# Optimization experiments

Hardware: AMD Instinct MI355X
Metric: run time of the kernel (lower is better)

The kernel has to match this reference:

```python
import jax, jax.numpy as jnp
import numpy as np

B, N, T, IN_DIM, OUT_DIM = 16, 500, 12, 2, 2
H, D, K, NH, NBLOCKS, T_OUT, GDEP = 64, 64, 10, 24, 2, 12, 2
H2 = 2 * H


def setup_inputs():
    key = jax.random.key(0)
    ks = iter(jax.random.split(key, 64))

    def rn(shape, s=1.0):
        return jax.random.normal(next(ks), shape, dtype=jnp.float32) * s

    def z(*shape):
        return jnp.zeros(shape, jnp.float32)

    sI = 1.0 / np.sqrt(IN_DIM)
    sH = 1.0 / np.sqrt(H)
    sH2 = 1.0 / np.sqrt(H2)
    sD = 1.0 / np.sqrt(D)
    adj = jax.random.uniform(next(ks), (N, N), dtype=jnp.float32)
    inp = {
        'x': rn((B, N, T, IN_DIM)),
        'weather': rn((B, T, 4)),
        'geo_adj': adj / adj.sum(1, keepdims=True),
        'fcx_W': rn((IN_DIM, H), sI), 'fcx_b': z(H),
        'env_cb': rn((K, D)), 'nodes_cb': rn((N, D)),
        'w_v': rn((D, K), sD), 'w_k': rn((D, D), sD), 'w_q': rn((D, D), sD),
        'core_W': rn((H, H * H), sH), 'core_b': z(H * H),
        'tcnN_Win': rn((K, H2, H2), sH2), 'tcnN_bin': z(K, H2),
        'tcnN_Wf': rn((K, NBLOCKS, 2, H2, H2), sH2), 'tcnN_bf': z(K, NBLOCKS, H2),
        'tcnN_Wg': rn((K, NBLOCKS, 2, H2, H2), sH2), 'tcnN_bg': z(K, NBLOCKS, H2),
        'tcnN_Wout': rn((K, H2, H), sH2), 'tcnN_bout': z(K, H),
        'tcnP_Win': rn((K, H2, H2), sH2), 'tcnP_bin': z(K, H2),
        'tcnP_Wf': rn((K, NBLOCKS, 2, H2, H2), sH2), 'tcnP_bf': z(K, NBLOCKS, H2),
        'tcnP_Wg': rn((K, NBLOCKS, 2, H2, H2), sH2), 'tcnP_bg': z(K, NBLOCKS, H2),
        'tcnP_Wout': rn((K, H2, H), sH2), 'tcnP_bout': z(K, H),
        'bn1_g': jnp.ones((H,), jnp.float32), 'bn1_b': z(H),
        'bnP_g': jnp.ones((H,), jnp.float32), 'bnP_b': z(H),
        'gcn1_W': rn((H, H), sH), 'gcn1_b': z(H),
        'gcn2_W': rn((H, H), sH), 'gcn2_b': z(H),
        'gcnp_W': rn((H, H), sH), 'gcnp_b': z(H),
        'nv_p1': rn((2 * NH, H)), 'nv_p2': rn((N, H)), 'nv_p3': rn((N, H)),
        'nv_pk': rn((H, H, H), sH),
        'out_W1': rn((T_OUT, H, 100), sH), 'out_b1': z(T_OUT, 100),
        'out_W2': rn((T_OUT, 100, OUT_DIM), 0.1), 'out_b2': z(T_OUT, OUT_DIM),
        't_pos': jax.random.randint(next(ks), (B, T, 2), 0, 7),
        'ind': jax.random.randint(next(ks), (B, T, 2), 0, 7),
    }
    return inp


def _tstep_emb(t, dim):
    half = dim // 2
    freqs = jnp.exp(-jnp.log(10000.0) * jnp.arange(half, dtype=jnp.float32) / half)
    a = t.astype(jnp.float32)[:, None] * freqs[None]
    return jnp.concatenate([jnp.cos(a), jnp.sin(a)], -1)


def _conv2(h, W, b, d):
    # causal kernel-2 dilated conv over time: h [B,N,T,C], W [2,C,Co] -> [B,N,T-d,Co]
    return (jnp.einsum('bntc,co->bnto', h[:, :, :-d], W[0])
            + jnp.einsum('bntc,co->bnto', h[:, :, d:], W[1]) + b)


def _tcn(xin, Win, bin_, Wf, bf, Wg, bg, Wout, bout):
    # gated dilated TCN (Graph-WaveNet style), per node over time
    h = jnp.einsum('bntc,co->bnto', xin, Win) + bin_
    for l in range(Wf.shape[0]):
        d = 2 ** l
        f = jnp.tanh(_conv2(h, Wf[l], bf[l], d))
        g = jax.nn.sigmoid(_conv2(h, Wg[l], bg[l], d))
        h = f * g + h[:, :, d:, :]
    return jnp.einsum('bntc,ch->bnth', h, Wout) + bout


def _bn(h, g, b):
    # BatchNorm1d over channels, stats over (batch, nodes); training mode
    mu = h.mean((0, 1))
    var = h.var((0, 1))
    return g * (h - mu) * jax.lax.rsqrt(var + 1e-5) + b


def _gcn(h, adj, W, b):
    # multi-hop diffusion: sum_{k=0..GDEP} A^k h, then linear
    eq = 'nm,bmh->bnh' if adj.ndim == 2 else 'bnm,bmh->bnh'
    acc, zt = h, h
    for _ in range(GDEP):
        zt = jnp.einsum(eq, adj, zt)
        acc = acc + zt
    return jnp.einsum('bnh,ho->bno', acc, W) + b


def _forward(x, weather, geo_adj, fcx_W, fcx_b, env_cb, nodes_cb, w_v, w_k, w_q,
             core_W, core_b,
             tcnN_Win, tcnN_bin, tcnN_Wf, tcnN_bf, tcnN_Wg, tcnN_bg, tcnN_Wout, tcnN_bout,
             tcnP_Win, tcnP_bin, tcnP_Wf, tcnP_bf, tcnP_Wg, tcnP_bg, tcnP_Wout, tcnP_bout,
             bn1_g, bn1_b, bnP_g, bnP_b, gcn1_W, gcn1_b, gcn2_W, gcn2_b, gcnp_W, gcnp_b,
             nv_p1, nv_p2, nv_p3, nv_pk, out_W1, out_b1, out_W2, out_b2, t_pos, ind):
    scale = 1.0 / jnp.sqrt(jnp.float32(D))
    ind_p = jnp.where(ind[:, :, 0] <= 4, ind[:, :, 1], NH - 1 + ind[:, :, 1])
    tp = jnp.where(t_pos[:, :, 0] <= 4, t_pos[:, :, 1], NH - 1 + t_pos[:, :, 1])
    t_emb = _tstep_emb(tp.reshape(-1), H).reshape(B, T, H)

    # codebook attention -> hard cluster assignment (gumbel softmax, straight-through)
    mat_v = env_cb @ w_v
    mat_k = env_cb @ w_k
    mat_q = nodes_cb @ w_q
    scores = jax.nn.softmax((mat_q @ mat_k.T) * scale, axis=1)
    logits = scores @ mat_v                                   # [N,K]
    gn = jax.random.gumbel(jax.random.key(42), logits.shape, dtype=logits.dtype)
    y_soft = jax.nn.softmax(logits + gn, axis=1)
    hard = jax.nn.one_hot(jnp.argmax(y_soft, axis=1), K, dtype=y_soft.dtype)
    mask = y_soft + jax.lax.stop_gradient(hard - y_soft)      # [N,K] one-hot fwd

    x_emb = jnp.einsum('bnti,ih->bnth', x, fcx_W) + fcx_b
    total_x = jnp.concatenate(
        [x_emb, jnp.broadcast_to(t_emb[:, None], (B, N, T, H))], -1)  # [B,N,T,2H]

    unbias = jnp.zeros((B, N, H), total_x.dtype)
    h_prev = jnp.zeros((B, N, H), total_x.dtype)
    for i in range(K):  # small fixed cluster count
        m = mask[:, i]
        xm = total_x * m[None, :, None, None]
        hn = _tcn(xm[:, :, 1:], tcnN_Win[i], tcnN_bin[i], tcnN_Wf[i], tcnN_bf[i],
                  tcnN_Wg[i], tcnN_bg[i], tcnN_Wout[i], tcnN_bout[i])[:, :, 0, :]
        hp = _tcn(xm[:, :, :-1], tcnP_Win[i], tcnP_bin[i], tcnP_Wf[i], tcnP_bf[i],
                  tcnP_Wg[i], tcnP_bg[i], tcnP_Wout[i], tcnP_bout[i])[:, :, 0, :]
        unbias = unbias + m[None, :, None] * hn
        h_prev = h_prev + m[None, :, None] * hp

    unbias = _bn(unbias, bn1_g, bn1_b)
    h_prev = _bn(h_prev, bnP_g, bnP_b)

    h1 = _gcn(h_prev, geo_adj, gcn1_W, gcn1_b)
    core = (t_emb[:, T - 1] @ core_W + core_b).reshape(B, H, H)
    causal = jax.nn.softmax(jnp.einsum('bnh,bhk,bmk->bnm', unbias, core, h_prev), axis=-1)
    h2 = _gcn(unbias, causal, gcn2_W, gcn2_b)

    te = nv_p1[ind_p[:, -(T - 1)]]                            # [B,H]
    adp = jnp.einsum('ai,ijk->ajk', te, nv_pk)
    adp = jnp.einsum('bj,ajk->abk', nv_p2, adp)
    adp = jnp.einsum('ck,abk->abc', nv_p3, adp)
    adp = jax.nn.softmax(jax.nn.relu(adp), axis=2)            # [B,N,N]
    h3 = _gcn(unbias, adp, gcnp_W, gcnp_b)

    cur_h = h1 + h2 + h3
    hmid = jax.nn.elu(jnp.einsum('bnh,thf->bntf', cur_h, out_W1) + out_b1)
    return jnp.einsum('bntf,tfo->bnto', hmid, out_W2) + out_b2  # [B,N,T_OUT,OUT_DIM]


def reference(x, weather, geo_adj, fcx_W, fcx_b, env_cb, nodes_cb, w_v, w_k, w_q,
              core_W, core_b,
              tcnN_Win, tcnN_bin, tcnN_Wf, tcnN_bf, tcnN_Wg, tcnN_bg, tcnN_Wout, tcnN_bout,
              tcnP_Win, tcnP_bin, tcnP_Wf, tcnP_bf, tcnP_Wg, tcnP_bg, tcnP_Wout, tcnP_bout,
              bn1_g, bn1_b, bnP_g, bnP_b, gcn1_W, gcn1_b, gcn2_W, gcn2_b, gcnp_W, gcnp_b,
              nv_p1, nv_p2, nv_p3, nv_pk, out_W1, out_b1, out_W2, out_b2, t_pos, ind):
    return _forward(x, weather, geo_adj, fcx_W, fcx_b, env_cb, nodes_cb, w_v, w_k, w_q,
                    core_W, core_b,
                    tcnN_Win, tcnN_bin, tcnN_Wf, tcnN_bf, tcnN_Wg, tcnN_bg, tcnN_Wout, tcnN_bout,
                    tcnP_Win, tcnP_bin, tcnP_Wf, tcnP_bf, tcnP_Wg, tcnP_bg, tcnP_Wout, tcnP_bout,
                    bn1_g, bn1_b, bnP_g, bnP_b, gcn1_W, gcn1_b, gcn2_W, gcn2_b, gcnp_W, gcnp_b,
                    nv_p1, nv_p2, nv_p3, nv_pk, out_W1, out_b1, out_W2, out_b2, t_pos, ind)
```

## Files before the change

kernel.cpp:

```cpp
#include <hip/hip_runtime.h>
#include <hip/hip_bf16.h>
#include <math.h>

#define B_ 16
#define N_ 500
#define T_ 12
#define K_ 10
#define NROWS (B_*N_)
#define TROWS 6
#define NTCN2 2688

__device__ __forceinline__ unsigned rotl32(unsigned v, int r){ return (v<<r)|(v>>(32-r)); }

__device__ __forceinline__ void threefry2x32(unsigned k0, unsigned k1,
                                             unsigned c0, unsigned c1,
                                             unsigned &o0, unsigned &o1){
  unsigned ks2 = k0 ^ k1 ^ 0x1BD11BDAu;
  unsigned x0 = c0 + k0, x1 = c1 + k1;
#define TF_R(r) { x0 += x1; x1 = rotl32(x1,(r)); x1 ^= x0; }
  TF_R(13) TF_R(15) TF_R(26) TF_R(6)
  x0 += k1;  x1 += ks2 + 1u;
  TF_R(17) TF_R(29) TF_R(16) TF_R(24)
  x0 += ks2; x1 += k0 + 2u;
  TF_R(13) TF_R(15) TF_R(26) TF_R(6)
  x0 += k0;  x1 += k1 + 3u;
  TF_R(17) TF_R(29) TF_R(16) TF_R(24)
  x0 += k1;  x1 += ks2 + 4u;
  TF_R(13) TF_R(15) TF_R(26) TF_R(6)
  x0 += ks2; x1 += k0 + 5u;
#undef TF_R
  o0 = x0; o1 = x1;
}

__device__ __forceinline__ float gumbel_at(unsigned idx){
  unsigned b0, b1;
  threefry2x32(0u, 42u, 0u, idx, b0, b1);
  unsigned bits = b0 ^ b1;
  float u = __uint_as_float((bits >> 9) | 0x3f800000u) - 1.0f;
  u = fmaxf(u, 1.17549435e-38f);
  return -logf(-logf(u));
}

__global__ __launch_bounds__(256) void k_matq(const float* __restrict__ nodes_cb,
                                              const float* __restrict__ w_q,
                                              float* __restrict__ matq){
  int idx = blockIdx.x*256 + threadIdx.x;
  if (idx >= N_*64) return;
  int n = idx >> 6, d = idx & 63;
  float a = 0.f;
  for (int c = 0; c < 64; ++c) a += nodes_cb[n*64+c] * w_q[c*64+d];
  matq[idx] = a;
}

__global__ __launch_bounds__(256) void k_route(const float* __restrict__ env_cb,
                                               const float* __restrict__ w_v,
                                               const float* __restrict__ w_k,
                                               const float* __restrict__ matq,
                                               int* __restrict__ node_list,
                                               int* __restrict__ off){
  __shared__ float smk[K_*64];
  __shared__ float smv[K_*K_];
  __shared__ int sroute[N_];
  int tid = threadIdx.x;
  for (int idx = tid; idx < K_*64; idx += 256){
    int kk = idx >> 6, d = idx & 63;
    float a = 0.f;
    for (int c = 0; c < 64; ++c) a += env_cb[kk*64+c] * w_k[c*64+d];
    smk[idx] = a;
  }
  for (int idx = tid; idx < K_*K_; idx += 256){
    int kk = idx / K_, j = idx % K_;
    float a = 0.f;
    for (int c = 0; c < 64; ++c) a += env_cb[kk*64+c] * w_v[c*K_+j];
    smv[idx] = a;
  }
  __syncthreads();
  for (int n = tid; n < N_; n += 256){
    float s[K_];
    float mx = -1e30f;
    for (int j = 0; j < K_; ++j){
      float a = 0.f;
      for (int d = 0; d < 64; ++d) a += matq[n*64+d]*smk[j*64+d];
      s[j] = a * 0.125f;
      mx = fmaxf(mx, s[j]);
    }
    float sum = 0.f;
    for (int j = 0; j < K_; ++j){ s[j] = expf(s[j]-mx); sum += s[j]; }
    float inv = 1.f/sum;
    int best = 0; float bestv = -1e30f;
    for (int j2 = 0; j2 < K_; ++j2){
      float lg = 0.f;
      for (int j = 0; j < K_; ++j) lg += s[j]*inv*smv[j*K_+j2];
      float tot = lg + gumbel_at((unsigned)(n*K_+j2));
      if (tot > bestv){ bestv = tot; best = j2; }
    }
    sroute[n] = best;
  }
  __syncthreads();
  if (tid == 0){
    int cnt[K_]; for (int j=0;j<K_;++j) cnt[j]=0;
    for (int n=0;n<N_;++n) cnt[sroute[n]]++;
    int acc=0;
    for (int j=0;j<K_;++j){ off[j]=acc; acc+=cnt[j]; }
    off[K_]=acc;
    int pos[K_]; for (int j=0;j<K_;++j) pos[j]=off[j];
    for (int n=0;n<N_;++n) node_list[pos[sroute[n]]++] = n;
    int* chunkOff = off + 16;
    int ck = 0;
    chunkOff[0] = 0;
    for (int s = 0; s < 2*K_; ++s){
      int rows = cnt[s >> 1] * 16;
      ck += (rows + TROWS - 1) / TROWS;
      chunkOff[s+1] = ck;
    }
  }
}

__global__ void k_temb(const int* __restrict__ t_pos, float* __restrict__ temb){
  int tid = threadIdx.x;
  if (tid >= B_*T_) return;
  int b = tid / T_, t = tid % T_;
  int p0 = t_pos[(b*T_+t)*2+0], p1 = t_pos[(b*T_+t)*2+1];
  float tp = (float)((p0 <= 4) ? p1 : 23 + p1);
  float c0 = -logf(10000.f)/32.f;
  for (int j = 0; j < 32; ++j){
    float a = tp * expf(c0 * (float)j);
    temb[(b*T_+t)*64 + j]      = cosf(a);
    temb[(b*T_+t)*64 + 32 + j] = sinf(a);
  }
}

__global__ __launch_bounds__(256) void k_core(const float* __restrict__ temb,
                                              const float* __restrict__ core_W,
                                              const float* __restrict__ core_b,
                                              float* __restrict__ core_f){
  int idx = blockIdx.x*256 + threadIdx.x;
  if (idx >= B_*4096) return;
  int b = idx >> 12, c = idx & 4095;
  const float* te = temb + (b*T_ + 11)*64;
  float a = core_b[c];
  for (int h = 0; h < 64; ++h) a += te[h] * core_W[h*4096 + c];
  core_f[idx] = a;
}

__global__ __launch_bounds__(256) void k_tmp1(const int* __restrict__ ind,
                                              const float* __restrict__ nv_p1,
                                              const float* __restrict__ nv_pk,
                                              float* __restrict__ tmp1){
  int idx = blockIdx.x*256 + threadIdx.x;
  if (idx >= B_*4096) return;
  int b = idx >> 12, c = idx & 4095;
  int i0 = ind[(b*T_+1)*2+0], i1 = ind[(b*T_+1)*2+1];
  int row = (i0 <= 4) ? i1 : 23 + i1;
  const float* te = nv_p1 + row*64;
  float a = 0.f;
  for (int h = 0; h < 64; ++h) a += te[h] * nv_pk[h*4096 + c];
  tmp1[idx] = a;
}

__global__ __launch_bounds__(128) void k_tprep(
    const float* __restrict__ temb,
    const float* __restrict__ fcx_W, const float* __restrict__ fcx_b,
    const float* __restrict__ WinN, const float* __restrict__ WinP,
    float* __restrict__ TE)
{
  int slot = blockIdx.x;
  int y = blockIdx.y;
  int k = slot >> 1, path = slot & 1;
  const float* Win = (path ? WinP : WinN) + k*16384;
  int o = threadIdx.x;
  if (y < 80){
    __shared__ float ste[64];
    int b = y/5, t = y%5;
    if (o < 64) ste[o] = temb[(b*T_ + t)*64 + o];
    __syncthreads();
    float acc = 0.f;
    for (int cc = 0; cc < 64; ++cc) acc += ste[cc] * Win[(64+cc)*128 + o];
    TE[slot*10240 + y*128 + o] = acc;
  } else {
    float a0=0.f, a1=0.f, c0=0.f;
    for (int c = 0; c < 64; ++c){
      float w = Win[c*128 + o];
      a0 += fcx_W[c]*w; a1 += fcx_W[64+c]*w; c0 += fcx_b[c]*w;
    }
    float* AAs = TE + 20*10240 + slot*384;
    AAs[o] = a0; AAs[128+o] = a1; AAs[256+o] = c0;
  }
}

__global__ __launch_bounds__(256) void k_tcn2(
    const float* __restrict__ x,
    const float* __restrict__ TE,
    const int* __restrict__ node_list, const int* __restrict__ off,
    const float* __restrict__ binN,
    const float* __restrict__ WfN,  const float* __restrict__ bfN,
    const float* __restrict__ WgN,  const float* __restrict__ bgN,
    const float* __restrict__ WoutN,const float* __restrict__ boutN,
    const float* __restrict__ binP,
    const float* __restrict__ WfP,  const float* __restrict__ bfP,
    const float* __restrict__ WgP,  const float* __restrict__ bgP,
    const float* __restrict__ WoutP,const float* __restrict__ boutP,
    float* __restrict__ out_unb, float* __restrict__ out_hpr)
{
  const int* chunkOff = off + 16;
  int nwork = chunkOff[2*K_];
  int q = (nwork + 7) >> 3;
  int id = blockIdx.x;
  int xcd = id & 7, pos = id >> 3;
  if (pos >= q) return;
  int w = xcd*q + pos;
  if (w >= nwork) return;
  int slot = 0;
  #pragma unroll 1
  while (chunkOff[slot+1] <= w) ++slot;
  int r0 = (w - chunkOff[slot]) * TROWS;

  int k = slot >> 1;
  int path = slot & 1;
  int cnt = off[k+1] - off[k];
  int rows = cnt * 16;
  if (r0 >= rows) return;

  const float* bin  = (path ? binP  : binN)  + k*128;
  const float* Wf   = (path ? WfP   : WfN)   + k*4*16384;
  const float* bf_  = (path ? bfP   : bfN)   + k*2*128;
  const float* Wg   = (path ? WgP   : WgN)   + k*4*16384;
  const float* bg_  = (path ? bgP   : bgN)   + k*2*128;
  const float* Wout = (path ? WoutP : WoutN) + k*8192;
  const float* bout = (path ? boutP : boutN) + k*64;
  float* outb = path ? out_hpr : out_unb;
  int t0 = path ? 0 : 1;

  __shared__ __align__(16) float sH0[TROWS*512];
  __shared__ __align__(16) float sH1[TROWS*256];
  __shared__ __align__(16) float sH2[TROWS*128];
  __shared__ float xs[TROWS][4][2];
  __shared__ int rowBN[TROWS];
  __shared__ int rowB[TROWS];

  int tid = threadIdx.x;
  if (tid < TROWS){
    int r = r0 + tid;
    if (r < rows){
      int node = node_list[off[k] + (r >> 4)];
      int b = r & 15;
      rowBN[tid] = b*N_ + node;
      rowB[tid]  = b;
    } else { rowBN[tid] = -1; rowB[tid] = 0; }
  }
  __syncthreads();
  if (tid < TROWS*4){
    int i = tid >> 2, tl = tid & 3;
    int rb = rowBN[i];
    float x0 = 0.f, x1 = 0.f;
    if (rb >= 0){
      const float* xp = x + (rb*T_ + tl + t0)*2;
      x0 = xp[0]; x1 = xp[1];
    }
    xs[i][tl][0] = x0; xs[i][tl][1] = x1;
  }
  __syncthreads();

  {
    int o = tid & 127, half = tid >> 7;
    const float* AAs = TE + 20*10240 + slot*384;
    const float* TEs = TE + slot*10240;
    float a0 = AAs[o], a1 = AAs[128+o], c0 = AAs[256+o];
    float bn = bin[o];
    #pragma unroll
    for (int jj = 0; jj < 12; ++jj){
      int rt = half*12 + jj;
      int i = rt >> 2, tl = rt & 3;
      float v = xs[i][tl][0]*a0 + xs[i][tl][1]*a1 + c0
              + TEs[(rowB[i]*5 + tl + t0)*128 + o] + bn;
      sH0[rt*128 + o] = v;
    }
  }
  __syncthreads();

  {
    int o = tid & 127;
    int jg = (tid >> 7)*6;
    float af[6], ag[6];
    #pragma unroll
    for (int j=0;j<6;++j){ af[j]=0.f; ag[j]=0.f; }
    for (int c = 0; c < 128; c += 4){
      float f00=Wf[(c+0)*128+o], f01=Wf[(c+1)*128+o], f02=Wf[(c+2)*128+o], f03=Wf[(c+3)*128+o];
      float f10=Wf[16384+(c+0)*128+o], f11=Wf[16384+(c+1)*128+o], f12=Wf[16384+(c+2)*128+o], f13=Wf[16384+(c+3)*128+o];
      float g00=Wg[(c+0)*128+o], g01=Wg[(c+1)*128+o], g02=Wg[(c+2)*128+o], g03=Wg[(c+3)*128+o];
      float g10=Wg[16384+(c+0)*128+o], g11=Wg[16384+(c+1)*128+o], g12=Wg[16384+(c+2)*128+o], g13=Wg[16384+(c+3)*128+o];
      #pragma unroll
      for (int jj=0;jj<6;++jj){
        int j = jg + jj;
        int i = j >> 1, ti = j & 1;
        float4 xa = *(const float4*)&sH0[(i*4+ti*2  )*128 + c];
        float4 xb = *(const float4*)&sH0[(i*4+ti*2+1)*128 + c];
        af[jj] += xa.x*f00 + xa.y*f01 + xa.z*f02 + xa.w*f03
                + xb.x*f10 + xb.y*f11 + xb.z*f12 + xb.w*f13;
        ag[jj] += xa.x*g00 + xa.y*g01 + xa.z*g02 + xa.w*g03
                + xb.x*g10 + xb.y*g11 + xb.z*g12 + xb.w*g13;
      }
    }
    float bfv = bf_[o], bgv = bg_[o];
    #pragma unroll
    for (int jj=0;jj<6;++jj){
      int j = jg + jj;
      int i = j >> 1, ti = j & 1;
      float f = tanhf(af[jj] + bfv);
      float g = 1.f/(1.f + expf(-(ag[jj] + bgv)));
      sH1[j*128 + o] = f*g + sH0[(i*4 + ti*2 + 1)*128 + o];
// ... 352 lines not shown
      int mm = fidx >> 4, k4 = (fidx & 15)*4;
      if (AMODE != 0){
        const float* kp = (AMODE == 1) ? &Keysf[(b*N_+mm)*64+k4] : &Keysb[mm*64+k4];
        float4 kv = *(const float4*)kp;
        kbuf[mm][k4+0]=kv.x; kbuf[mm][k4+1]=kv.y; kbuf[mm][k4+2]=kv.z; kbuf[mm][k4+3]=kv.w;
      }
      *(float4*)&xbuf[mm][k4] = *(const float4*)&X[(b*N_+mm)*64+k4];
    }
    if (AMODE == 0){
      int r = tid >> 4, m4 = (tid & 15)*4;
      int nn = n0 + r;
      float4 g0 = (nn < N_) ? *(const float4*)&geo[nn*N_ + m4] : f40;
      *(float4*)&pbuf[r][m4] = g0;
    }
    __syncthreads();
  }

  float m_runA = -1e30f, l_runA = 0.f;
  float m_runB = -1e30f, l_runB = 0.f;
  float accA[4] = {0.f,0.f,0.f,0.f};
  float accB[4] = {0.f,0.f,0.f,0.f};

  for (int ci = 0; ci < 8; ++ci){
    int m0 = ci*64;
    if (ci < 7){
      #pragma unroll
      for (int ii=0; ii<4; ++ii){
        int fidx = tid + ii*256;
        int mm = fidx >> 4, k4 = (fidx & 15)*4;
        int m = m0 + 64 + mm;
        if (AMODE != 0){
          if (m < N_){
            const float* kp = (AMODE == 1) ? &Keysf[(b*N_+m)*64+k4] : &Keysb[m*64+k4];
            rrK4[ii] = *(const float4*)kp;
          } else rrK4[ii] = f40;
        }
        rrX4[ii] = (m < N_) ? *(const float4*)&X[(b*N_+m)*64+k4] : f40;
      }
      if (AMODE == 0){
        int r = tid >> 4, m4 = (tid & 15)*4;
        int nn = n0 + r, m = m0 + 64 + m4;
        rrA4 = (nn < N_ && m < N_) ? *(const float4*)&geo[nn*N_ + m] : f40;
      }
    }
    if (AMODE != 0){
      float s0A = 0.f, s1A = 0.f, s0B = 0.f, s1B = 0.f;
      for (int kk = 0; kk < 64; kk += 4){
        float4 qA = *(const float4*)&vbuf[nl  ][kk];
        float4 qB = *(const float4*)&vbuf[nl+8][kk];
        float4 k0 = *(const float4*)&kbuf[ml   ][kk];
        float4 k1 = *(const float4*)&kbuf[ml+32][kk];
        s0A += qA.x*k0.x + qA.y*k0.y + qA.z*k0.z + qA.w*k0.w;
        s1A += qA.x*k1.x + qA.y*k1.y + qA.z*k1.z + qA.w*k1.w;
        s0B += qB.x*k0.x + qB.y*k0.y + qB.z*k0.z + qB.w*k0.w;
        s1B += qB.x*k1.x + qB.y*k1.y + qB.z*k1.z + qB.w*k1.w;
      }
      float v0A = (m0 + ml      < N_) ? (RELU ? fmaxf(s0A, 0.f) : s0A) : -1e30f;
      float v1A = (m0 + ml + 32 < N_) ? (RELU ? fmaxf(s1A, 0.f) : s1A) : -1e30f;
      float v0B = (m0 + ml      < N_) ? (RELU ? fmaxf(s0B, 0.f) : s0B) : -1e30f;
      float v1B = (m0 + ml + 32 < N_) ? (RELU ? fmaxf(s1B, 0.f) : s1B) : -1e30f;
      float cmaxA = fmaxf(v0A, v1A), cmaxB = fmaxf(v0B, v1B);
      #pragma unroll
      for (int msk = 1; msk < 32; msk <<= 1){
        cmaxA = fmaxf(cmaxA, __shfl_xor(cmaxA, msk, 32));
        cmaxB = fmaxf(cmaxB, __shfl_xor(cmaxB, msk, 32));
      }
      float mnewA = fmaxf(m_runA, cmaxA), mnewB = fmaxf(m_runB, cmaxB);
      float scaleA = expf(m_runA - mnewA), scaleB = expf(m_runB - mnewB);
      float p0A = expf(v0A - mnewA), p1A = expf(v1A - mnewA);
      float p0B = expf(v0B - mnewB), p1B = expf(v1B - mnewB);
      float lcA = p0A + p1A, lcB = p0B + p1B;
      #pragma unroll
      for (int msk = 1; msk < 32; msk <<= 1){
        lcA += __shfl_xor(lcA, msk, 32);
        lcB += __shfl_xor(lcB, msk, 32);
      }
      l_runA = l_runA*scaleA + lcA; m_runA = mnewA;
      l_runB = l_runB*scaleB + lcB; m_runB = mnewB;
      #pragma unroll
      for (int d=0; d<4; ++d){ accA[d] *= scaleA; accB[d] *= scaleB; }
      pbuf[nl  ][ml]    = p0A;
      pbuf[nl  ][ml+32] = p1A;
      pbuf[nl+8][ml]    = p0B;
      pbuf[nl+8][ml+32] = p1B;
    }
    __syncthreads();
    #pragma unroll
    for (int mm = 0; mm < 32; mm += 4){
      float4 pA = *(const float4*)&pbuf[nl  ][mh + mm];
      float4 pB = *(const float4*)&pbuf[nl+8][mh + mm];
      float4 x0 = *(const float4*)&xbuf[mh+mm+0][d0];
      float4 x1 = *(const float4*)&xbuf[mh+mm+1][d0];
      float4 x2 = *(const float4*)&xbuf[mh+mm+2][d0];
      float4 x3 = *(const float4*)&xbuf[mh+mm+3][d0];
      accA[0] += pA.x*x0.x + pA.y*x1.x + pA.z*x2.x + pA.w*x3.x;
      accA[1] += pA.x*x0.y + pA.y*x1.y + pA.z*x2.y + pA.w*x3.y;
      accA[2] += pA.x*x0.z + pA.y*x1.z + pA.z*x2.z + pA.w*x3.z;
      accA[3] += pA.x*x0.w + pA.y*x1.w + pA.z*x2.w + pA.w*x3.w;
      accB[0] += pB.x*x0.x + pB.y*x1.x + pB.z*x2.x + pB.w*x3.x;
      accB[1] += pB.x*x0.y + pB.y*x1.y + pB.z*x2.y + pB.w*x3.y;
      accB[2] += pB.x*x0.z + pB.y*x1.z + pB.z*x2.z + pB.w*x3.z;
      accB[3] += pB.x*x0.w + pB.y*x1.w + pB.z*x2.w + pB.w*x3.w;
    }
    __syncthreads();
    if (ci < 7){
      #pragma unroll
      for (int ii=0; ii<4; ++ii){
        int fidx = tid + ii*256;
        int mm = fidx >> 4, k4 = (fidx & 15)*4;
        if (AMODE != 0){
          float4 kv = rrK4[ii];
          kbuf[mm][k4+0]=kv.x; kbuf[mm][k4+1]=kv.y; kbuf[mm][k4+2]=kv.z; kbuf[mm][k4+3]=kv.w;
        }
        *(float4*)&xbuf[mm][k4] = rrX4[ii];
      }
      if (AMODE == 0){
        int r = tid >> 4, m4 = (tid & 15)*4;
        *(float4*)&pbuf[r][m4] = rrA4;
      }
      __syncthreads();
    }
  }
  #pragma unroll
  for (int d=0; d<4; ++d){
    accA[d] += __shfl_xor(accA[d], 16, 32);
    accB[d] += __shfl_xor(accB[d], 16, 32);
  }
  if (AMODE != 0){
    float invA = 1.f / l_runA, invB = 1.f / l_runB;
    #pragma unroll
    for (int d=0; d<4; ++d){ accA[d] *= invA; accB[d] *= invB; }
  }

  if (!FINAL){
    if (ml < 16){
      if (nA < N_){
        float4 o4; o4.x = accA[0]; o4.y = accA[1]; o4.z = accA[2]; o4.w = accA[3];
        *(float4*)&Y[(b*N_+nA)*64 + d0] = o4;
      }
      if (nB < N_){
        float4 o4; o4.x = accB[0]; o4.y = accB[1]; o4.z = accB[2]; o4.w = accB[3];
        *(float4*)&Y[(b*N_+nB)*64 + d0] = o4;
      }
    }
    return;
  }

  {
    if (ml < 16){
      float4 svA = {0.f,0.f,0.f,0.f}, svB = {0.f,0.f,0.f,0.f};
      if (nA < N_){
        int row = b*N_ + nA;
        float4 x0v = *(const float4*)&X0[row*64 + d0];
        float4 z1v = *(const float4*)&Z1[row*64 + d0];
        svA.x = accA[0] + x0v.x + z1v.x;
        svA.y = accA[1] + x0v.y + z1v.y;
        svA.z = accA[2] + x0v.z + z1v.z;
        svA.w = accA[3] + x0v.w + z1v.w;
      }
      if (nB < N_){
        int row = b*N_ + nB;
        float4 x0v = *(const float4*)&X0[row*64 + d0];
        float4 z1v = *(const float4*)&Z1[row*64 + d0];
        svB.x = accB[0] + x0v.x + z1v.x;
        svB.y = accB[1] + x0v.y + z1v.y;
        svB.z = accB[2] + x0v.z + z1v.z;
        svB.w = accB[3] + x0v.w + z1v.w;
      }
      *(float4*)&vbuf[nl  ][d0] = svA;
      *(float4*)&vbuf[nl+8][d0] = svB;
    }
    #pragma unroll
    for (int ii = 0; ii < 4; ++ii){
      int fidx = tid + ii*256;
      int r = fidx >> 4, k4 = (fidx & 15)*4;
      float4 wv = *(const float4*)&Wg[r*64 + k4];
      kbuf[r][k4+0]=wv.x; kbuf[r][k4+1]=wv.y; kbuf[r][k4+2]=wv.z; kbuf[r][k4+3]=wv.w;
    }
    __syncthreads();
    float oxA = 0.f, oyA = 0.f, oxB = 0.f, oyB = 0.f;
    for (int kk = 0; kk < 64; ++kk){
      float sA = vbuf[nl][kk], sB = vbuf[nl+8][kk];
      float2 w2 = *(const float2*)&kbuf[kk][ml*2];
      oxA += sA*w2.x; oyA += sA*w2.y;
      oxB += sB*w2.x; oyB += sB*w2.y;
    }
    float2 bv = *(const float2*)&bg[ml*2];
    if (nA < N_){
      int row = b*N_ + nA;
      float vx = oxA + bv.x, vy = oyA + bv.y;
      if (ADD){
        float2 old = *(const float2*)&cur[row*64 + ml*2];
        vx += old.x; vy += old.y;
      }
      float2 o2; o2.x = vx; o2.y = vy;
      *(float2*)&cur[row*64 + ml*2] = o2;
    }
    if (nB < N_){
      int row = b*N_ + nB;
      float vx = oxB + bv.x, vy = oyB + bv.y;
      if (ADD){
        float2 old = *(const float2*)&cur[row*64 + ml*2];
        vx += old.x; vy += old.y;
      }
      float2 o2; o2.x = vx; o2.y = vy;
      *(float2*)&cur[row*64 + ml*2] = o2;
    }
  }
}

template<int AMODE, int RELU>
__global__ __launch_bounds__(256) void k_attn_p1(
    const float* __restrict__ Qf, const float* __restrict__ Qb,
    const float* __restrict__ M,
    const float* __restrict__ Keysf, const float* __restrict__ Keysb,
    const float* __restrict__ X,
    float* __restrict__ Pb, float* __restrict__ Y)
{
  __shared__ __align__(16) float kbuf[64][65];
  __shared__ __align__(16) float xbuf[64][64];
  __shared__ __align__(16) float vbuf[16][64];
  __shared__ __align__(16) float pbuf[16][64];

  int b = blockIdx.y, n0 = blockIdx.x*16;
  int tid = threadIdx.x;
  int nl = tid >> 5, ml = tid & 31;
  int nA = n0 + nl, nB = n0 + nl + 8;
  int mh = (ml >> 4) << 5;
  int d0 = (ml & 15) * 4;
  const float4 f40 = {0.f,0.f,0.f,0.f};
  float4 rrK4[4], rrX4[4];

  {
    int r = tid >> 4, k4 = (tid & 15) * 4;
    int nn = n0 + r;
    float4 qv = f40;
    if (nn < N_){
      const float* qp = (AMODE == 1) ? &Qf[(b*N_+nn)*64+k4] : &Qb[nn*64+k4];
      qv = *(const float4*)qp;
    }
    *(float4*)&pbuf[r][k4] = qv;
  }
  #pragma unroll
  for (int ii = 0; ii < 4; ++ii){
    int fidx = tid + ii*256;
    int r = fidx >> 4, k4 = (fidx & 15)*4;
    float4 v = *(const float4*)&M[b*4096 + r*64 + k4];
    kbuf[r][k4+0]=v.x; kbuf[r][k4+1]=v.y; kbuf[r][k4+2]=v.z; kbuf[r][k4+3]=v.w;
  }
  __syncthreads();
  float vxA = 0.f, vyA = 0.f, vxB = 0.f, vyB = 0.f;
  for (int kk = 0; kk < 64; ++kk){
    float qA = pbuf[nl][kk], qB = pbuf[nl+8][kk];
    float2 m2 = *(const float2*)&kbuf[kk][ml*2];
    vxA += qA*m2.x; vyA += qA*m2.y;
    vxB += qB*m2.x; vyB += qB*m2.y;
  }
  __syncthreads();
  vbuf[nl  ][ml*2] = vxA; vbuf[nl  ][ml*2+1] = vyA;
  vbuf[nl+8][ml*2] = vxB; vbuf[nl+8][ml*2+1] = vyB;
  __syncthreads();
  #pragma unroll
  for (int ii = 0; ii < 4; ++ii){
    int fidx = tid + ii*256;
    int mm = fidx >> 4, k4 = (fidx & 15)*4;
    const float* kp = (AMODE == 1) ? &Keysf[(b*N_+mm)*64+k4] : &Keysb[mm*64+k4];
    float4 kv = *(const float4*)kp;
    kbuf[mm][k4+0]=kv.x; kbuf[mm][k4+1]=kv.y; kbuf[mm][k4+2]=kv.z; kbuf[mm][k4+3]=kv.w;
    *(float4*)&xbuf[mm][k4] = *(const float4*)&X[(b*N_+mm)*64+k4];
  }
  __syncthreads();

  float m_runA = -1e30f, l_runA = 0.f;
  float m_runB = -1e30f, l_runB = 0.f;
  float accA[4] = {0.f,0.f,0.f,0.f};
  float accB[4] = {0.f,0.f,0.f,0.f};

  for (int ci = 0; ci < 8; ++ci){
    int m0 = ci*64;
    if (ci < 7){
      #pragma unroll
      for (int ii=0; ii<4; ++ii){
        int fidx = tid + ii*256;
        int mm = fidx >> 4, k4 = (fidx & 15)*4;
        int m = m0 + 64 + mm;
        if (m < N_){
          const float* kp = (AMODE == 1) ? &Keysf[(b*N_+m)*64+k4] : &Keysb[m*64+k4];
          rrK4[ii] = *(const float4*)kp;
          rrX4[ii] = *(const float4*)&X[(b*N_+m)*64+k4];
        } else { rrK4[ii] = f40; rrX4[ii] = f40; }
      }
    }
    {
      float s0A = 0.f, s1A = 0.f, s0B = 0.f, s1B = 0.f;
      for (int kk = 0; kk < 64; kk += 4){
        float4 qA = *(const float4*)&vbuf[nl  ][kk];
        float4 qB = *(const float4*)&vbuf[nl+8][kk];
        float4 k0 = *(const float4*)&kbuf[ml   ][kk];
        float4 k1 = *(const float4*)&kbuf[ml+32][kk];
        s0A += qA.x*k0.x + qA.y*k0.y + qA.z*k0.z + qA.w*k0.w;
        s1A += qA.x*k1.x + qA.y*k1.y + qA.z*k1.z + qA.w*k1.w;
        s0B += qB.x*k0.x + qB.y*k0.y + qB.z*k0.z + qB.w*k0.w;
        s1B += qB.x*k1.x + qB.y*k1.y + qB.z*k1.z + qB.w*k1.w;
      }
      float v0A = (m0 + ml      < N_) ? (RELU ? fmaxf(s0A, 0.f) : s0A) : -1e30f;
      float v1A = (m0 + ml + 32 < N_) ? (RELU ? fmaxf(s1A, 0.f) : s1A) : -1e30f;
      float v0B = (m0 + ml      < N_) ? (RELU ? fmaxf(s0B, 0.f) : s0B) : -1e30f;
      float v1B = (m0 + ml + 32 < N_) ? (RELU ? fmaxf(s1B, 0.f) : s1B) : -1e30f;
      if (nA < N_){
        Pb[((long)(b*N_+nA))*512 + m0 + ml]      = v0A;
        Pb[((long)(b*N_+nA))*512 + m0 + ml + 32] = v1A;
      }
      if (nB < N_){
        Pb[((long)(b*N_+nB))*512 + m0 + ml]      = v0B;
        Pb[((long)(b*N_+nB))*512 + m0 + ml + 32] = v1B;
      }
      float cmaxA = fmaxf(v0A, v1A), cmaxB = fmaxf(v0B, v1B);
      #pragma unroll
      for (int msk = 1; msk < 32; msk <<= 1){
        cmaxA = fmaxf(cmaxA, __shfl_xor(cmaxA, msk, 32));
// ... 204 lines not shown
        svB.y = accB[1] + x0v.y + z1v.y;
        svB.z = accB[2] + x0v.z + z1v.z;
        svB.w = accB[3] + x0v.w + z1v.w;
      }
      *(float4*)&vbuf[nl  ][d0] = svA;
      *(float4*)&vbuf[nl+8][d0] = svB;
    }
    #pragma unroll
    for (int ii=0; ii<4; ++ii){
      int fidx = tid + ii*256;
      int r = fidx >> 4, k4 = (fidx & 15)*4;
      *(float4*)&xbuf[r][k4] = *(const float4*)&Wg[r*64 + k4];
    }
    __syncthreads();
    float oxA = 0.f, oyA = 0.f, oxB = 0.f, oyB = 0.f;
    for (int kk = 0; kk < 64; ++kk){
      float sA = vbuf[nl][kk], sB = vbuf[nl+8][kk];
      float2 w2 = *(const float2*)&xbuf[kk][ml*2];
      oxA += sA*w2.x; oyA += sA*w2.y;
      oxB += sB*w2.x; oyB += sB*w2.y;
    }
    float2 bv = *(const float2*)&bg[ml*2];
    if (nA < N_){
      int row = b*N_ + nA;
      float vx = oxA + bv.x, vy = oyA + bv.y;
      if (ADD){
        float2 old = *(const float2*)&cur[row*64 + ml*2];
        vx += old.x; vy += old.y;
      }
      float2 o2; o2.x = vx; o2.y = vy;
      *(float2*)&cur[row*64 + ml*2] = o2;
    }
    if (nB < N_){
      int row = b*N_ + nB;
      float vx = oxB + bv.x, vy = oyB + bv.y;
      if (ADD){
        float2 old = *(const float2*)&cur[row*64 + ml*2];
        vx += old.x; vy += old.y;
      }
      float2 o2; o2.x = vx; o2.y = vy;
      *(float2*)&cur[row*64 + ml*2] = o2;
    }
  }
}

__global__ __launch_bounds__(128) void k_out(const float* __restrict__ cur,
                                             const float* __restrict__ W1, const float* __restrict__ bb1,
                                             const float* __restrict__ W2, const float* __restrict__ bb2,
                                             float* __restrict__ out){
  __shared__ float ch[8][64];
  __shared__ float hid[8*1200];
  int tid = threadIdx.x;
  int rbase = blockIdx.x*8;
  for (int idx = tid; idx < 512; idx += 128){
    int r = idx >> 6, h = idx & 63;
    ch[r][h] = cur[(rbase+r)*64 + h];
  }
  __syncthreads();
  for (int job = tid; job < 1200; job += 128){
    int t = job / 100, f = job - t*100;
    float bb = bb1[t*100+f];
    float a0=bb,a1=bb,a2=bb,a3=bb,a4=bb,a5=bb,a6=bb,a7=bb;
    for (int h = 0; h < 64; ++h){
      float w = W1[(t*64+h)*100 + f];
      a0 += ch[0][h]*w; a1 += ch[1][h]*w; a2 += ch[2][h]*w; a3 += ch[3][h]*w;
      a4 += ch[4][h]*w; a5 += ch[5][h]*w; a6 += ch[6][h]*w; a7 += ch[7][h]*w;
    }
    hid[0*1200+job] = (a0 > 0.f) ? a0 : expm1f(a0);
    hid[1*1200+job] = (a1 > 0.f) ? a1 : expm1f(a1);
    hid[2*1200+job] = (a2 > 0.f) ? a2 : expm1f(a2);
    hid[3*1200+job] = (a3 > 0.f) ? a3 : expm1f(a3);
    hid[4*1200+job] = (a4 > 0.f) ? a4 : expm1f(a4);
    hid[5*1200+job] = (a5 > 0.f) ? a5 : expm1f(a5);
    hid[6*1200+job] = (a6 > 0.f) ? a6 : expm1f(a6);
    hid[7*1200+job] = (a7 > 0.f) ? a7 : expm1f(a7);
  }
  __syncthreads();
  for (int jb = tid; jb < 192; jb += 128){
    int r = jb / 24, rem = jb % 24;
    int t = rem >> 1, o = rem & 1;
    float a = bb2[t*2+o];
    const float* hp = hid + r*1200 + t*100;
    for (int f = 0; f < 100; ++f) a += hp[f] * W2[(t*100+f)*2+o];
    out[(rbase+r)*24 + t*2+o] = a;
  }
}

extern "C" void kernel_launch(void* const* d_in, const int* in_sizes, int n_in,
                              void* d_out, int out_size, void* d_ws, size_t ws_size,
                              hipStream_t stream)
{
  const float* x        = (const float*)d_in[0];
  const float* geo      = (const float*)d_in[2];
  const float* fcx_W    = (const float*)d_in[3];
  const float* fcx_b    = (const float*)d_in[4];
  const float* env_cb   = (const float*)d_in[5];
  const float* nodes_cb = (const float*)d_in[6];
  const float* w_v      = (const float*)d_in[7];
  const float* w_k      = (const float*)d_in[8];
  const float* w_q      = (const float*)d_in[9];
  const float* core_W   = (const float*)d_in[10];
  const float* core_b   = (const float*)d_in[11];
  const float* tN_Win   = (const float*)d_in[12];
  const float* tN_bin   = (const float*)d_in[13];
  const float* tN_Wf    = (const float*)d_in[14];
  const float* tN_bf    = (const float*)d_in[15];
  const float* tN_Wg    = (const float*)d_in[16];
  const float* tN_bg    = (const float*)d_in[17];
  const float* tN_Wout  = (const float*)d_in[18];
  const float* tN_bout  = (const float*)d_in[19];
  const float* tP_Win   = (const float*)d_in[20];
  const float* tP_bin   = (const float*)d_in[21];
  const float* tP_Wf    = (const float*)d_in[22];
  const float* tP_bf    = (const float*)d_in[23];
  const float* tP_Wg    = (const float*)d_in[24];
  const float* tP_bg    = (const float*)d_in[25];
  const float* tP_Wout  = (const float*)d_in[26];
  const float* tP_bout  = (const float*)d_in[27];
  const float* bn1_g    = (const float*)d_in[28];
  const float* bn1_b    = (const float*)d_in[29];
  const float* bnP_g    = (const float*)d_in[30];
  const float* bnP_b    = (const float*)d_in[31];
  const float* gcn1_W   = (const float*)d_in[32];
  const float* gcn1_b   = (const float*)d_in[33];
  const float* gcn2_W   = (const float*)d_in[34];
  const float* gcn2_b   = (const float*)d_in[35];
  const float* gcnp_W   = (const float*)d_in[36];
  const float* gcnp_b   = (const float*)d_in[37];
  const float* nv_p1    = (const float*)d_in[38];
  const float* nv_p2    = (const float*)d_in[39];
  const float* nv_p3    = (const float*)d_in[40];
  const float* nv_pk    = (const float*)d_in[41];
  const float* out_W1   = (const float*)d_in[42];
  const float* out_b1   = (const float*)d_in[43];
  const float* out_W2   = (const float*)d_in[44];
  const float* out_b2   = (const float*)d_in[45];
  const int*   t_pos    = (const int*)d_in[46];
  const int*   ind      = (const int*)d_in[47];

  int* node_list = (int*)d_ws;
  int* off       = node_list + 512;
  float* F = (float*)((char*)d_ws + 4096);
  float* temb   = F + 0;
  float* core_f = F + 12288;
  float* tmp1   = F + 77824;
  float* stats  = F + 143360;
  float* matq   = F + 143616;
  float* unb    = F + 175616;
  float* hpr    = F + 687616;
  float* cur    = F + 1199616;
  float* zt1    = F + 1711616;
  float* Pb     = F + 2223616;
  float* TE     = Pb;
  bool useP = ws_size >= (size_t)(4096 + (size_t)(2223616 + 4096000)*4);

  k_matq <<<dim3(125), dim3(256), 0, stream>>>(nodes_cb, w_q, matq);
  k_route<<<dim3(1),   dim3(256), 0, stream>>>(env_cb, w_v, w_k, matq, node_list, off);
  k_temb <<<dim3(1),   dim3(192), 0, stream>>>(t_pos, temb);
  k_core <<<dim3(256), dim3(256), 0, stream>>>(temb, core_W, core_b, core_f);
  if (useP){
    k_tprep<<<dim3(20, 81), dim3(128), 0, stream>>>(temb, fcx_W, fcx_b, tN_Win, tP_Win, TE);
    k_tcn2 <<<dim3(NTCN2), dim3(256), 0, stream>>>(x, TE, node_list, off,
        tN_bin, tN_Wf, tN_bf, tN_Wg, tN_bg, tN_Wout, tN_bout,
        tP_bin, tP_Wf, tP_bf, tP_Wg, tP_bg, tP_Wout, tP_bout,
        unb, hpr);
  } else {
    k_tcn  <<<dim3(20, 334), dim3(256), 0, stream>>>(x, fcx_W, fcx_b, temb, node_list, off,
        tN_Win, tN_bin, tN_Wf, tN_bf, tN_Wg, tN_bg, tN_Wout, tN_bout,
        tP_Win, tP_bin, tP_Wf, tP_bf, tP_Wg, tP_bg, tP_Wout, tP_bout,
        unb, hpr);
  }
  k_bnstats<<<dim3(128), dim3(256), 0, stream>>>(unb, hpr, stats);
  k_bnapply<<<dim3(1000),dim3(256), 0, stream>>>(unb, hpr, stats, bn1_g, bn1_b, bnP_g, bnP_b);
  k_tmp1<<<dim3(256), dim3(256), 0, stream>>>(ind, nv_p1, nv_pk, tmp1);

  dim3 ag(32, 16);
  const float* nil = nullptr;
  k_attn<0,0,0,0><<<ag, 256, 0, stream>>>(geo, nil,nil,nil, nil,nil,
                                 hpr, nil,nil, nil,nil, nullptr, zt1);
  k_attn<0,0,1,0><<<ag, 256, 0, stream>>>(geo, nil,nil,nil, nil,nil,
                                 zt1, hpr, zt1, gcn1_W, gcn1_b, cur, nullptr);
  if (useP){
    k_attn_p1<1,0><<<ag, 256, 0, stream>>>(unb, nil, core_f, hpr, nil, unb, Pb, zt1);
    k_attn_p2<1>  <<<ag, 256, 0, stream>>>(Pb, zt1, unb, gcn2_W, gcn2_b, cur);
  } else {
    k_attn<1,0,0,0><<<ag, 256, 0, stream>>>(nil, unb,nil, core_f, hpr,nil,
                                   unb, nil,nil, nil,nil, nullptr, zt1);
    k_attn<1,0,1,1><<<ag, 256, 0, stream>>>(nil, unb,nil, core_f, hpr,nil,
                                   zt1, unb, zt1, gcn2_W, gcn2_b, cur, nullptr);
  }
  if (useP){
    k_attn_p1<2,1><<<ag, 256, 0, stream>>>(nil, nv_p2, tmp1, nil, nv_p3, unb, Pb, zt1);
    k_attn_p2<1>  <<<ag, 256, 0, stream>>>(Pb, zt1, unb, gcnp_W, gcnp_b, cur);
  } else {
    k_attn<2,1,0,0><<<ag, 256, 0, stream>>>(nil, nil,nv_p2, tmp1, nil,nv_p3,
                                   unb, nil,nil, nil,nil, nullptr, zt1);
    k_attn<2,1,1,1><<<ag, 256, 0, stream>>>(nil, nil,nv_p2, tmp1, nil,nv_p3,
                                   zt1, unb, zt1, gcnp_W, gcnp_b, cur, nullptr);
  }
  k_out<<<dim3(1000), dim3(128), 0, stream>>>(cur, out_W1, out_b1, out_W2, out_b2, (float*)d_out);
}
```

Baseline: 835.0 us.

## Precompute geo_adj plus its square to fuse two graph propagation passes

Adds a kernel that computes G + G·G once from the geo adjacency (input-independent of activations but computed per call). The first GCN stage then does a single propagation with this combined matrix plus the gcn1 projection, replacing two sequential attention/propagation launches. The FINAL==2 path skips the Z1 residual load. This trades one batched propagation for an N^3 matrix product each call and changes the floating-point summation order.

New measurement: 852.9 us. +2.1%, slower.

```diff
diff --git a/kernel.cpp b/kernel.cpp
--- a/kernel.cpp
+++ b/kernel.cpp
@@ -156,6 +156,40 @@
   float a = 0.f;
   for (int h = 0; h < 64; ++h) a += te[h] * nv_pk[h*4096 + c];
   tmp1[idx] = a;
+}
+
+__global__ __launch_bounds__(256) void k_geo2(const float* __restrict__ geo,
+                                              float* __restrict__ gsum){
+  __shared__ float srow[4][512];
+  int n0 = blockIdx.x*4;
+  int tid = threadIdx.x;
+  for (int idx = tid; idx < 2048; idx += 256){
+    int r = idx >> 9, k = idx & 511;
+    srow[r][k] = (n0 + r < N_ && k < N_) ? geo[(n0+r)*N_ + k] : 0.f;
+  }
+  __syncthreads();
+  float acc0[4] = {0.f,0.f,0.f,0.f};
+  float acc1[4] = {0.f,0.f,0.f,0.f};
+  int m0 = tid, m1 = tid + 256;
+  bool v1 = (m1 < N_);
+  for (int k = 0; k < N_; ++k){
+    float g0 = geo[k*N_ + m0];
+    float g1 = v1 ? geo[k*N_ + m1] : 0.f;
+    #pragma unroll
+    for (int r = 0; r < 4; ++r){
+      float a = srow[r][k];
+      acc0[r] += a*g0;
+      acc1[r] += a*g1;
+    }
+  }
+  #pragma unroll
+  for (int r = 0; r < 4; ++r){
+    int n = n0 + r;
+    if (n < N_){
+      gsum[n*N_+m0] = geo[n*N_+m0] + acc0[r];
+      if (v1) gsum[n*N_+m1] = geo[n*N_+m1] + acc1[r];
+    }
+  }
 }
 
 __global__ __launch_bounds__(128) void k_tprep(
@@ -814,20 +848,26 @@
       if (nA < N_){
         int row = b*N_ + nA;
         float4 x0v = *(const float4*)&X0[row*64 + d0];
-        float4 z1v = *(const float4*)&Z1[row*64 + d0];
-        svA.x = accA[0] + x0v.x + z1v.x;
-        svA.y = accA[1] + x0v.y + z1v.y;
-        svA.z = accA[2] + x0v.z + z1v.z;
-        svA.w = accA[3] + x0v.w + z1v.w;
+        svA.x = accA[0] + x0v.x;
+        svA.y = accA[1] + x0v.y;
+        svA.z = accA[2] + x0v.z;
+        svA.w = accA[3] + x0v.w;
+        if (FINAL == 1){
+          float4 z1v = *(const float4*)&Z1[row*64 + d0];
+          svA.x += z1v.x; svA.y += z1v.y; svA.z += z1v.z; svA.w += z1v.w;
+        }
       }
       if (nB < N_){
         int row = b*N_ + nB;
         float4 x0v = *(const float4*)&X0[row*64 + d0];
-        float4 z1v = *(const float4*)&Z1[row*64 + d0];
-        svB.x = accB[0] + x0v.x + z1v.x;
-        svB.y = accB[1] + x0v.y + z1v.y;
-        svB.z = accB[2] + x0v.z + z1v.z;
-        svB.w = accB[3] + x0v.w + z1v.w;
+        svB.x = accB[0] + x0v.x;
+        svB.y = accB[1] + x0v.y;
+        svB.z = accB[2] + x0v.z;
+        svB.w = accB[3] + x0v.w;
+        if (FINAL == 1){
+          float4 z1v = *(const float4*)&Z1[row*64 + d0];
+          svB.x += z1v.x; svB.y += z1v.y; svB.z += z1v.z; svB.w += z1v.w;
+        }
       }
       *(float4*)&vbuf[nl  ][d0] = svA;
       *(float4*)&vbuf[nl+8][d0] = svB;
@@ -1338,6 +1378,7 @@
   float* zt1    = F + 1711616;
   float* Pb     = F + 2223616;
   float* TE     = Pb;
+  float* Gsum   = zt1;
   bool useP = ws_size >= (size_t)(4096 + (size_t)(2223616 + 4096000)*4);
 
   k_matq <<<dim3(125), dim3(256), 0, stream>>>(nodes_cb, w_q, matq);
@@ -1350,6 +1391,7 @@
         tN_bin, tN_Wf, tN_bf, tN_Wg, tN_bg, tN_Wout, tN_bout,
         tP_bin, tP_Wf, tP_bf, tP_Wg, tP_bg, tP_Wout, tP_bout,
         unb, hpr);
+    k_geo2 <<<dim3(125), dim3(256), 0, stream>>>(geo, Gsum);
   } else {
     k_tcn  <<<dim3(20, 334), dim3(256), 0, stream>>>(x, fcx_W, fcx_b, temb, node_list, off,
         tN_Win, tN_bin, tN_Wf, tN_bf, tN_Wg, tN_bg, tN_Wout, tN_bout,
@@ -1362,10 +1404,15 @@
 
   dim3 ag(32, 16);
   const float* nil = nullptr;
-  k_attn<0,0,0,0><<<ag, 256, 0, stream>>>(geo, nil,nil,nil, nil,nil,
-                                 hpr, nil,nil, nil,nil, nullptr, zt1);
-  k_attn<0,0,1,0><<<ag, 256, 0, stream>>>(geo, nil,nil,nil, nil,nil,
-                                 zt1, hpr, zt1, gcn1_W, gcn1_b, cur, nullptr);
+  if (useP){
+    k_attn<0,0,2,0><<<ag, 256, 0, stream>>>(Gsum, nil,nil,nil, nil,nil,
+                                   hpr, hpr, nil, gcn1_W, gcn1_b, cur, nullptr);
+  } else {
+    k_attn<0,0,0,0><<<ag, 256, 0, stream>>>(geo, nil,nil,nil, nil,nil,
+                                   hpr, nil,nil, nil,nil, nullptr, zt1);
+    k_attn<0,0,1,0><<<ag, 256, 0, stream>>>(geo, nil,nil,nil, nil,nil,
+                                   zt1, hpr, zt1, gcn1_W, gcn1_b, cur, nullptr);
+  }
   if (useP){
     k_attn_p1<1,0><<<ag, 256, 0, stream>>>(unb, nil, core_f, hpr, nil, unb, Pb, zt1);
     k_attn_p2<1>  <<<ag, 256, 0, stream>>>(Pb, zt1, unb, gcn2_W, gcn2_b, cur);
```
